# Optimization experiments

Measured on AMD Instinct MI355X. Metric: run time of the kernel, lower is better.

Reference implementation:

```python
import jax, jax.numpy as jnp
import numpy as np

HEADS = 16

def setup_inputs() -> dict:
    key = jax.random.key(0)
    k1, k2, k3 = jax.random.split(key, 3)
    B, N, C = 4, 4096, 1024
    x = jax.random.normal(k1, (B, N, C), dtype=jnp.float32)
    w_qkv = jax.random.normal(k2, (3 * C, C), dtype=jnp.float32) * (C ** -0.5)
    w_proj = jax.random.normal(k3, (C, C), dtype=jnp.float32) * (C ** -0.5)
    b_proj = jnp.zeros((C,), dtype=jnp.float32)
    return {"x": x, "w_qkv": w_qkv, "w_proj": w_proj, "b_proj": b_proj}

def reference(x, w_qkv, w_proj, b_proj):
    B, N, C = x.shape
    H = HEADS
    D = C // H
    qkv = x @ w_qkv.T                      # [B,N,3C]
    q, k, v = jnp.split(qkv, 3, axis=-1)   # each [B,N,C]
    # b n (h d) -> b h d n
    def to_bhdn(t):
        return t.reshape(B, N, H, D).transpose(0, 2, 3, 1)
    q = jax.nn.relu(to_bhdn(q))
    k = jax.nn.relu(to_bhdn(k))
    v = to_bhdn(v)
    eps = jnp.finfo(q.dtype).eps
    ksum = k.sum(axis=-1)                                   # [B,H,D]
    z = 1.0 / (jnp.einsum('bhd,bhdn->bhn', ksum, q) + eps)  # [B,H,N]
    context = jnp.einsum('bhdn,bhen->bhde', v, k)            # v @ k^T, [B,H,D,D]
    out = jnp.einsum('bhde,bhen->bhdn', context, q)          # [B,H,D,N]
    out = out * z[:, :, None, :]
    # b h d n -> b n (h d)
    out = out.transpose(0, 3, 1, 2).reshape(B, N, C)
    return out @ w_proj.T + b_proj
```

## Files before the change

### kernel.cpp

```cpp
#include <hip/hip_runtime.h>
#include <hip/hip_bf16.h>


typedef __bf16 bf16;
typedef __bf16 bf16x8 __attribute__((ext_vector_type(8)));
typedef __bf16 bf16x4 __attribute__((ext_vector_type(4)));
typedef float  f32x4  __attribute__((ext_vector_type(4)));

#define MFMA16(a, b, c) __builtin_amdgcn_mfma_f32_16x16x32_bf16((a), (b), (c), 0, 0, 0)

__device__ __forceinline__ void gload_lds16(const bf16* g, bf16* l) {
  __builtin_amdgcn_global_load_lds(
      (const __attribute__((address_space(1))) void*)g,
      (__attribute__((address_space(3))) void*)l, 16, 0, 0);
}

__global__ __launch_bounds__(256) void cvt3(const float* __restrict__ x,  bf16* __restrict__ xb,
                                            const float* __restrict__ wq, bf16* __restrict__ wqb,
                                            const float* __restrict__ wp, bf16* __restrict__ wpb) {
  const long stride = (long)gridDim.x * 256;
  for (long i4 = (long)blockIdx.x * 256 + threadIdx.x; i4 < 5242880; i4 += stride) {
    const float* s; bf16* d; long off;
    if (i4 < 4194304)      { s = x;  d = xb;  off = i4; }
    else if (i4 < 4980736) { s = wq; d = wqb; off = i4 - 4194304; }
    else                   { s = wp; d = wpb; off = i4 - 4980736; }
    const float4 v = *(const float4*)(s + off * 4);
    bf16x4 o;
    o[0] = (bf16)v.x; o[1] = (bf16)v.y; o[2] = (bf16)v.z; o[3] = (bf16)v.w;
    *(bf16x4*)(d + off * 4) = o;
  }
}

template <int LDC, typename CO>
__global__ __launch_bounds__(256) void gemm_bt(const bf16* __restrict__ A,
                                               const bf16* __restrict__ Bm,
                                               CO* __restrict__ Co,
                                               const float* __restrict__ bias,
                                               const int reluRows) {
  __shared__ bf16 As[128 * 32];
  __shared__ bf16 Bs[128 * 32];
  const int tid  = threadIdx.x;
  const int lane = tid & 63;
  const int w    = tid >> 6;
  const int wr   = w >> 1;
  const int wc   = w & 1;
  const int i0 = blockIdx.y * 128;
  const int j0 = blockIdx.x * 128;

  const int srow = lane >> 2;
  const int scol = (lane & 3) * 8;
  const bf16* Ag = A  + (long)(i0 + w * 32 + srow) * 1024 + scol;
  const bf16* Bg = Bm + (long)(j0 + w * 32 + srow) * 1024 + scol;
  bf16* Asw = As + w * 32 * 32;
  bf16* Bsw = Bs + w * 32 * 32;

  const int r15  = lane & 15;
  const int koff = (lane >> 4) * 8;

  f32x4 acc[4][4] = {};

  for (int kk = 0; kk < 1024; kk += 32) {
    gload_lds16(Ag + kk,             Asw);
    gload_lds16(Ag + kk + 16 * 1024, Asw + 16 * 32);
    gload_lds16(Bg + kk,             Bsw);
    gload_lds16(Bg + kk + 16 * 1024, Bsw + 16 * 32);
    __syncthreads();
    bf16x8 af[4], bfm[4];
#pragma unroll
    for (int t = 0; t < 4; ++t)
      af[t] = *(const bf16x8*)(As + (wr * 64 + t * 16 + r15) * 32 + koff);
#pragma unroll
    for (int u = 0; u < 4; ++u)
      bfm[u] = *(const bf16x8*)(Bs + (wc * 64 + u * 16 + r15) * 32 + koff);
#pragma unroll
    for (int t = 0; t < 4; ++t)
#pragma unroll
      for (int u = 0; u < 4; ++u)
        acc[t][u] = MFMA16(af[t], bfm[u], acc[t][u]);
    __syncthreads();
  }

  const bool doRelu = (i0 < reluRows);
  const int rbase = i0 + wr * 64;
  const int cbase = j0 + wc * 64;
#pragma unroll
  for (int t = 0; t < 4; ++t) {
    const int r0 = rbase + t * 16 + (lane >> 4) * 4;
#pragma unroll
    for (int u = 0; u < 4; ++u) {
      const int cc = cbase + u * 16 + r15;
      const float bv = bias ? bias[cc] : 0.0f;
#pragma unroll
      for (int jj = 0; jj < 4; ++jj) {
        float v = acc[t][u][jj] + bv;
        if (doRelu) v = fmaxf(v, 0.0f);
        Co[(long)(r0 + jj) * LDC + cc] = (CO)v;
      }
    }
  }
}

__global__ __launch_bounds__(256) void ctx_kernel(const bf16* __restrict__ QKV,
                                                  float* __restrict__ ctx_part,
                                                  float* __restrict__ ksum_part) {
  __shared__ bf16 Kl[64 * 128];
  __shared__ bf16 Vl[64 * 128];
  const int bh = blockIdx.x;
  const int s  = blockIdx.y;
  const int b  = bh >> 4, h = bh & 15;
  const int tid = threadIdx.x, lane = tid & 63, w = tid >> 6;
  const long ldq = 16384;
  const bf16* Kp = QKV + (long)(1024 + h * 64) * ldq + b * 4096 + s * 512;
  const bf16* Vp = QKV + (long)(2048 + h * 64) * ldq + b * 4096 + s * 512;
  const int r15 = lane & 15, g = lane >> 4;
  const int x7 = r15 & 7;

  long soff[4]; int dofs[4];
#pragma unroll
  for (int j = 0; j < 4; ++j) {
    const int row = w * 16 + j * 4 + g;
    soff[j] = (long)row * ldq + ((lane & 15) ^ (row & 7)) * 8;
    dofs[j] = (w * 16 + j * 4) * 128;
  }
  const int vrow = (w * 16 + r15) * 128;

  bf16x8 ones;
#pragma unroll
  for (int i = 0; i < 8; ++i) ones[i] = (bf16)1.0f;

  f32x4 acc[4]   = {};
  f32x4 accks[4] = {};

  for (int cc = 0; cc < 4; ++cc) {
#pragma unroll
    for (int j = 0; j < 4; ++j) {
      gload_lds16(Kp + soff[j] + cc * 128, Kl + dofs[j]);
      gload_lds16(Vp + soff[j] + cc * 128, Vl + dofs[j]);
    }
    __syncthreads();
#pragma unroll
    for (int nk = 0; nk < 4; ++nk) {
      const int ch = ((nk * 4 + g) ^ x7) * 8;
      const bf16x8 av = *(const bf16x8*)(Vl + vrow + ch);
#pragma unroll
      for (int u = 0; u < 4; ++u) {
        const bf16x8 kb = *(const bf16x8*)(Kl + (u * 16 + r15) * 128 + ch);
        acc[u]   = MFMA16(av,   kb, acc[u]);
        accks[u] = MFMA16(ones, kb, accks[u]);
      }
    }
    __syncthreads();
  }

  float* cp = ctx_part + (long)(bh * 8 + s) * 4096;
#pragma unroll
  for (int u = 0; u < 4; ++u)
#pragma unroll
    for (int jj = 0; jj < 4; ++jj) {
      const int d = w * 16 + g * 4 + jj;
      const int e = u * 16 + r15;
      cp[d * 64 + e] = acc[u][jj];
    }
  if (w == 0 && g == 0) {
#pragma unroll
    for (int u = 0; u < 4; ++u)
      ksum_part[(bh * 8 + s) * 64 + u * 16 + r15] = accks[u][0];
  }
}

__global__ __launch_bounds__(256) void out_kernel(const bf16* __restrict__ QKV,
                                                  const float* __restrict__ ctx_part,
                                                  const float* __restrict__ ksum_part,
                                                  bf16* __restrict__ O) {
  __shared__ bf16 ctx_lds[64 * 88];
  __shared__ bf16 qlds[256 * 80];
  __shared__ float ksum_lds[64];
  __shared__ float zlds[256];

  const int bh = blockIdx.x;
  const int nc = blockIdx.y;
  const int b = bh >> 4, h = bh & 15;
  const int tid = threadIdx.x, lane = tid & 63, w = tid >> 6;
  const int n0 = nc * 256;
  const long ldq = 16384;

  const float* cp = ctx_part + (long)bh * 8 * 4096;
#pragma unroll
  for (int r = 0; r < 16; ++r) {
    const int idx = tid + r * 256;
    float v = 0.0f;
#pragma unroll
    for (int s2 = 0; s2 < 8; ++s2) v += cp[s2 * 4096 + idx];
    ctx_lds[(idx >> 6) * 88 + (idx & 63)] = (bf16)v;
  }
  if (tid < 64) {
    float v = 0.0f;
#pragma unroll
    for (int s2 = 0; s2 < 8; ++s2) v += ksum_part[(bh * 8 + s2) * 64 + tid];
    ksum_lds[tid] = v;
  }
  {
    const bf16* Qp = QKV + (long)(h * 64) * ldq + b * 4096 + n0;
    const int e = tid >> 2, seg = tid & 3;
    const bf16* qr = Qp + (long)e * ldq + seg * 64;
#pragma unroll
    for (int i = 0; i < 64; i += 8) {
      const bf16x8 v = *(const bf16x8*)(qr + i);
#pragma unroll
      for (int jj = 0; jj < 8; ++jj) qlds[(seg * 64 + i + jj) * 80 + e] = v[jj];
    }
  }
  __syncthreads();

  {
    float a = 0.0f;
    const bf16* qrow = qlds + tid * 80;
#pragma unroll
    for (int d = 0; d < 64; ++d) a += (float)qrow[d] * ksum_lds[d];
    zlds[tid] = 1.0f / (a + 1.1920929e-07f);
  }
  const int r15 = lane & 15;
  const int koff = (lane >> 4) * 8;
  bf16x8 afr[4][2];
#pragma unroll
  for (int t = 0; t < 4; ++t)
#pragma unroll
    for (int s2 = 0; s2 < 2; ++s2)
      afr[t][s2] = *(const bf16x8*)(ctx_lds + (t * 16 + r15) * 88 + s2 * 32 + koff);
  __syncthreads();

#pragma unroll
  for (int nt = 0; nt < 4; ++nt) {
    const int ntile = w * 4 + nt;
    bf16x8 bfr[2];
#pragma unroll
    for (int s2 = 0; s2 < 2; ++s2)
      bfr[s2] = *(const bf16x8*)(qlds + (ntile * 16 + r15) * 80 + s2 * 32 + koff);
    f32x4 accn[4] = {};
#pragma unroll
    for (int t = 0; t < 4; ++t) {
      accn[t] = MFMA16(afr[t][0], bfr[0], accn[t]);
      accn[t] = MFMA16(afr[t][1], bfr[1], accn[t]);
    }
    const int ncol = n0 + ntile * 16 + r15;
    const float zv = zlds[ntile * 16 + r15];
    bf16* orow = O + (long)(b * 4096 + ncol) * 1024 + h * 64;
#pragma unroll
    for (int t = 0; t < 4; ++t) {
      const int d0 = t * 16 + (lane >> 4) * 4;
      bf16x4 pk;
#pragma unroll
      for (int jj = 0; jj < 4; ++jj) pk[jj] = (bf16)(accn[t][jj] * zv);
      *(bf16x4*)(orow + d0) = pk;
    }
  }
}

template <int LDC, typename CO>
__global__ __launch_bounds__(512, 2) void gemm256(const bf16* __restrict__ A,
                                                  const bf16* __restrict__ Bm,
                                                  CO* __restrict__ Co,
                                                  const float* __restrict__ bias,
                                                  const int reluRows) {
  __shared__ bf16 As[2][256 * 64];
  __shared__ bf16 Bs[2][256 * 64];
  const int tid  = threadIdx.x;
  const int lane = tid & 63;
  const int w    = tid >> 6;
  const int wm   = w >> 2;
  const int wn   = w & 3;

  const int gx = gridDim.x, gy = gridDim.y;
  const int nwg = gx * gy;
  const int id  = blockIdx.x + gx * blockIdx.y;
  const int sid = (id & 7) * (nwg >> 3) + (id >> 3);
  int bx, by;
  if (gx < gy) { bx = sid % gx; by = sid / gx; }
  else         { by = sid % gy; bx = sid / gy; }
  const int i0 = by * 256;
  const int j0 = bx * 256;

  const int lr = lane >> 3;
  const int lc = (lane & 7) ^ lr;
  const bf16* Agl = A  + (long)(i0 + 8 * w + lr) * 1024 + lc * 8;
  const bf16* Bgl = Bm + (long)(j0 + 8 * w + lr) * 1024 + lc * 8;
  const int wofs = w * 512;

  const int r15 = lane & 15, g = lane >> 4;
  const int ck[2] = { ((0 + g) ^ (r15 & 7)) * 8, ((4 + g) ^ (r15 & 7)) * 8 };
  const int arow = (wm * 128 + r15) * 64;
  const int brow = (wn * 64 + r15) * 64;

  f32x4 acc[8][4] = {};

#pragma unroll
  for (int q = 0; q < 4; ++q) {
    gload_lds16(Agl + q * 65536, &As[0][q * 4096 + wofs]);
    gload_lds16(Bgl + q * 65536, &Bs[0][q * 4096 + wofs]);
  }

  for (int kt = 0; kt < 16; ++kt) {
    const int cur = kt & 1;
    if (kt < 15) {
      const long ko = (long)(kt + 1) * 64;
#pragma unroll
      for (int q = 0; q < 4; ++q) {
        gload_lds16(Agl + ko + q * 65536, &As[cur ^ 1][q * 4096 + wofs]);
        gload_lds16(Bgl + ko + q * 65536, &Bs[cur ^ 1][q * 4096 + wofs]);
      }
      asm volatile("s_waitcnt vmcnt(8)" ::: "memory");
    } else {
      asm volatile("s_waitcnt vmcnt(0)" ::: "memory");
    }
    __builtin_amdgcn_s_barrier();
    __builtin_amdgcn_sched_barrier(0);

    const bf16* Ab = &As[cur][arow];
    const bf16* Bb = &Bs[cur][brow];
#pragma unroll
    for (int ks = 0; ks < 2; ++ks) {
      bf16x8 af[8], bfr[4];
#pragma unroll
      for (int fm = 0; fm < 8; ++fm)
        af[fm] = *(const bf16x8*)(Ab + fm * 1024 + ck[ks]);
#pragma unroll
      for (int fn = 0; fn < 4; ++fn)
        bfr[fn] = *(const bf16x8*)(Bb + fn * 1024 + ck[ks]);
      __builtin_amdgcn_s_setprio(1);
#pragma unroll
      for (int fm = 0; fm < 8; ++fm)
#pragma unroll
        for (int fn = 0; fn < 4; ++fn)
          acc[fm][fn] = MFMA16(af[fm], bfr[fn], acc[fm][fn]);
      __builtin_amdgcn_s_setprio(0);
    }
    asm volatile("s_waitcnt lgkmcnt(0)" ::: "memory");
    __builtin_amdgcn_sched_barrier(0);
    __builtin_amdgcn_s_barrier();
  }

  const bool doRelu = (i0 < reluRows);
#pragma unroll
  for (int fm = 0; fm < 8; ++fm) {
    const int r0 = i0 + wm * 128 + fm * 16 + g * 4;
#pragma unroll
    for (int fn = 0; fn < 4; ++fn) {
      const int cc = j0 + wn * 64 + fn * 16 + r15;
      const float bv = bias ? bias[cc] : 0.0f;
#pragma unroll
      for (int jj = 0; jj < 4; ++jj) {
        float v = acc[fm][fn][jj] + bv;
        if (doRelu) v = fmaxf(v, 0.0f);
        Co[(long)(r0 + jj) * LDC + cc] = (CO)v;
      }
    }
  }
}

extern "C" void kernel_launch(void* const* d_in, const int* in_sizes, int n_in,
                              void* d_out, int out_size, void* d_ws, size_t ws_size,
                              hipStream_t stream) {
  const float* x      = (const float*)d_in[0];
  const float* w_qkv  = (const float*)d_in[1];
  const float* w_proj = (const float*)d_in[2];
  const float* b_proj = (const float*)d_in[3];
  float* out = (float*)d_out;

  char* ws = (char*)d_ws;
  bf16*  QKV       = (bf16*)ws;
  float* ctx_part  = (float*)(ws + 100663296);
  float* ksum_part = (float*)(ws + 100663296 + 8388608);
  bf16*  xb        = (bf16*)(ws + 109182976);
  bf16*  O         = xb;
  bf16*  wqkvb     = (bf16*)(ws + 109182976 + 33554432);
  bf16*  wprojb    = (bf16*)(ws + 109182976 + 33554432 + 6291456);

  cvt3<<<2048, 256, 0, stream>>>(x, xb, w_qkv, wqkvb, w_proj, wprojb);
  gemm_bt<16384, bf16><<<dim3(128, 24), 256, 0, stream>>>(wqkvb, xb, QKV, nullptr, 2048);
  ctx_kernel<<<dim3(64, 8), 256, 0, stream>>>(QKV, ctx_part, ksum_part);
  out_kernel<<<dim3(64, 16), 256, 0, stream>>>(QKV, ctx_part, ksum_part, O);
  gemm256<1024, float><<<dim3(4, 64), 512, 0, stream>>>(O, wprojb, out, b_proj, 0);
}
```

Baseline: 223.6 us.

## Triple-buffer QKV GEMM LDS tiles with async global-to-LDS prefetch

Converts the QKV projection GEMM from a single-buffered load/sync/compute loop into a 3-stage ring of LDS buffers. Tiles two steps ahead are prefetched with global_load_lds while MFMAs run on the current tile, gated by explicit vmcnt waits and raw s_barriers. This is meant to hide global memory latency behind compute, at the cost of three times the LDS footprint, which may lower occupancy. It also vectorizes the q·ksum dot product in out_kernel to use 8-wide bf16 LDS reads.

Measured after the change: 226.7 us. Within noise of the previous version (+1.4%).

```diff
diff --git a/kernel.cpp b/kernel.cpp
--- a/kernel.cpp
+++ b/kernel.cpp
@@ -32,13 +32,13 @@
 }
 
 template <int LDC, typename CO>
-__global__ __launch_bounds__(256) void gemm_bt(const bf16* __restrict__ A,
-                                               const bf16* __restrict__ Bm,
-                                               CO* __restrict__ Co,
-                                               const float* __restrict__ bias,
-                                               const int reluRows) {
-  __shared__ bf16 As[128 * 32];
-  __shared__ bf16 Bs[128 * 32];
+__global__ __launch_bounds__(256) void gemm_bt3(const bf16* __restrict__ A,
+                                                const bf16* __restrict__ Bm,
+                                                CO* __restrict__ Co,
+                                                const float* __restrict__ bias,
+                                                const int reluRows) {
+  __shared__ bf16 As[3][128 * 32];
+  __shared__ bf16 Bs[3][128 * 32];
   const int tid  = threadIdx.x;
   const int lane = tid & 63;
   const int w    = tid >> 6;
@@ -51,34 +51,59 @@
   const int scol = (lane & 3) * 8;
   const bf16* Ag = A  + (long)(i0 + w * 32 + srow) * 1024 + scol;
   const bf16* Bg = Bm + (long)(j0 + w * 32 + srow) * 1024 + scol;
-  bf16* Asw = As + w * 32 * 32;
-  bf16* Bsw = Bs + w * 32 * 32;
+  const int wofs = w * 1024;
 
   const int r15  = lane & 15;
   const int koff = (lane >> 4) * 8;
 
   f32x4 acc[4][4] = {};
 
-  for (int kk = 0; kk < 1024; kk += 32) {
-    gload_lds16(Ag + kk,             Asw);
-    gload_lds16(Ag + kk + 16 * 1024, Asw + 16 * 32);
-    gload_lds16(Bg + kk,             Bsw);
-    gload_lds16(Bg + kk + 16 * 1024, Bsw + 16 * 32);
-    __syncthreads();
+#define STG(kt, bsel)                                            \
+  do {                                                           \
+    const int kk_ = (kt) * 32;                                   \
+    gload_lds16(Ag + kk_,             &As[bsel][wofs]);          \
+    gload_lds16(Ag + kk_ + 16 * 1024, &As[bsel][wofs + 512]);    \
+    gload_lds16(Bg + kk_,             &Bs[bsel][wofs]);          \
+    gload_lds16(Bg + kk_ + 16 * 1024, &Bs[bsel][wofs + 512]);    \
+  } while (0)
+
+  STG(0, 0);
+  STG(1, 1);
+
+  int cur = 0, nxt = 2;
+  for (int kt = 0; kt < 32; ++kt) {
+    if (kt < 30) {
+      STG(kt + 2, nxt);
+      asm volatile("s_waitcnt vmcnt(8)" ::: "memory");
+    } else if (kt == 30) {
+      asm volatile("s_waitcnt vmcnt(4)" ::: "memory");
+    } else {
+      asm volatile("s_waitcnt vmcnt(0)" ::: "memory");
+    }
+    __builtin_amdgcn_s_barrier();
+    __builtin_amdgcn_sched_barrier(0);
+
+    const bf16* Ab = &As[cur][0];
+    const bf16* Bb = &Bs[cur][0];
     bf16x8 af[4], bfm[4];
 #pragma unroll
     for (int t = 0; t < 4; ++t)
-      af[t] = *(const bf16x8*)(As + (wr * 64 + t * 16 + r15) * 32 + koff);
+      af[t] = *(const bf16x8*)(Ab + (wr * 64 + t * 16 + r15) * 32 + koff);
 #pragma unroll
     for (int u = 0; u < 4; ++u)
-      bfm[u] = *(const bf16x8*)(Bs + (wc * 64 + u * 16 + r15) * 32 + koff);
+      bfm[u] = *(const bf16x8*)(Bb + (wc * 64 + u * 16 + r15) * 32 + koff);
 #pragma unroll
     for (int t = 0; t < 4; ++t)
 #pragma unroll
       for (int u = 0; u < 4; ++u)
         acc[t][u] = MFMA16(af[t], bfm[u], acc[t][u]);
-    __syncthreads();
-  }
+    __builtin_amdgcn_s_barrier();
+    __builtin_amdgcn_sched_barrier(0);
+
+    cur = (cur == 2) ? 0 : cur + 1;
+    nxt = (nxt == 2) ? 0 : nxt + 1;
+  }
+#undef STG
 
   const bool doRelu = (i0 < reluRows);
   const int rbase = i0 + wr * 64;
@@ -216,7 +241,11 @@
     float a = 0.0f;
     const bf16* qrow = qlds + tid * 80;
 #pragma unroll
-    for (int d = 0; d < 64; ++d) a += (float)qrow[d] * ksum_lds[d];
+    for (int d0 = 0; d0 < 64; d0 += 8) {
+      const bf16x8 qv = *(const bf16x8*)(qrow + d0);
+#pragma unroll
+      for (int jj = 0; jj < 8; ++jj) a += (float)qv[jj] * ksum_lds[d0 + jj];
+    }
     zlds[tid] = 1.0f / (a + 1.1920929e-07f);
   }
   const int r15 = lane & 15;
@@ -376,7 +405,7 @@
   bf16*  wprojb    = (bf16*)(ws + 109182976 + 33554432 + 6291456);
 
   cvt3<<<2048, 256, 0, stream>>>(x, xb, w_qkv, wqkvb, w_proj, wprojb);
-  gemm_bt<16384, bf16><<<dim3(128, 24), 256, 0, stream>>>(wqkvb, xb, QKV, nullptr, 2048);
+  gemm_bt3<16384, bf16><<<dim3(128, 24), 256, 0, stream>>>(wqkvb, xb, QKV, nullptr, 2048);
   ctx_kernel<<<dim3(64, 8), 256, 0, stream>>>(QKV, ctx_part, ksum_part);
   out_kernel<<<dim3(64, 16), 256, 0, stream>>>(QKV, ctx_part, ksum_part, O);
   gemm256<1024, float><<<dim3(4, 64), 512, 0, stream>>>(O, wprojb, out, b_proj, 0);
```
